# Performance work log

Measured on AMD Instinct MI355X. Metric: run time of the kernel, lower is better.

## Reference

```python
import jax, jax.numpy as jnp
import numpy as np

# Config (matches init_kwargs defaults): V=25 joints, C=16 -> D=400, heads=2,
# ffn=64*25=1600, window L=9, stride=1, postnorm, gelu, dropout ignored (eval).
N, C, T, V = 16, 16, 300, 25
D = C * V          # 400
H = 2              # nhead
FF = 64 * V        # 1600
L = 9              # trans_length
MAX_LEN = 301


def _layernorm(x, g, b, eps=1e-5):
    mu = jnp.mean(x, axis=-1, keepdims=True)
    var = jnp.mean(jnp.square(x - mu), axis=-1, keepdims=True)
    return (x - mu) * jax.lax.rsqrt(var + eps) * g + b


def setup_inputs() -> dict:
    key = jax.random.key(0)
    ks = jax.random.split(key, 12)
    s = 0.02
    return {
        "x": jax.random.normal(ks[0], (N, C, T, V), jnp.float32),
        "pe": jax.random.normal(ks[1], (1, MAX_LEN, D), jnp.float32) * s,
        "w_in": jax.random.normal(ks[2], (3 * D, D), jnp.float32) * s,
        "b_in": jnp.zeros((3 * D,), jnp.float32),
        "w_out": jax.random.normal(ks[3], (D, D), jnp.float32) * s,
        "b_out": jnp.zeros((D,), jnp.float32),
        "w1": jax.random.normal(ks[4], (FF, D), jnp.float32) * s,
        "b1": jnp.zeros((FF,), jnp.float32),
        "w2": jax.random.normal(ks[5], (D, FF), jnp.float32) * s,
        "b2": jnp.zeros((D,), jnp.float32),
        "ln1_g": jnp.ones((D,), jnp.float32),
        "ln1_b": jnp.zeros((D,), jnp.float32),
        "ln2_g": jnp.ones((D,), jnp.float32),
        "ln2_b": jnp.zeros((D,), jnp.float32),
    }


def _encoder_layer(h, w_in, b_in, w_out, b_out, w1, b1, w2, b2,
                   ln1_g, ln1_b, ln2_g, ln2_b):
    # h: [B, L, D]; post-norm TransformerEncoderLayer (torch default)
    B, Lw, Dm = h.shape
    dh = Dm // H
    qkv = h @ w_in.T + b_in                             # [B,L,3D]
    q, k, v = jnp.split(qkv, 3, axis=-1)
    def heads(t):
        return t.reshape(B, Lw, H, dh).transpose(0, 2, 1, 3)  # [B,H,L,dh]
    q, k, v = heads(q), heads(k), heads(v)
    scores = jnp.einsum('bhqd,bhkd->bhqk', q, k) / np.float32(np.sqrt(dh))
    att = jax.nn.softmax(scores, axis=-1)
    o = jnp.einsum('bhqk,bhkd->bhqd', att, v)
    o = o.transpose(0, 2, 1, 3).reshape(B, Lw, Dm) @ w_out.T + b_out
    h = _layernorm(h + o, ln1_g, ln1_b)
    ff = jax.nn.gelu(h @ w1.T + b1, approximate=False) @ w2.T + b2
    return _layernorm(h + ff, ln2_g, ln2_b)


def reference(x, pe, w_in, b_in, w_out, b_out, w1, b1, w2, b2,
              ln1_g, ln1_b, ln2_g, ln2_b):
    n, c, t, v = x.shape
    d = c * v
    # [N,C,T,V] -> [N,T,V,C] -> [N,T,D]  (flatten order is (V,C), as in torch view)
    xs = x.transpose(0, 2, 3, 1).reshape(n, t, d)
    xs = xs + pe[:, :t, :]
    W = t - L                                            # number of windows (stride=1)
    win = jnp.arange(W)
    idx = win[:, None] + jnp.arange(L)[None, :]          # [W,L] gather indices
    xw = xs[:, idx, :].reshape(n * W, L, d)              # batched windows
    out = _encoder_layer(xw, w_in, b_in, w_out, b_out, w1, b1, w2, b2,
                         ln1_g, ln1_b, ln2_g, ln2_b)
    out = out.reshape(n, W * L, d)
    # window i writes into rows i//2 : i//2 + L and results are summed
    pos = ((win // 2)[:, None] + jnp.arange(L)[None, :]).reshape(-1)  # [W*L]
    xt = jnp.zeros((n, t, d), xs.dtype).at[:, pos, :].add(out)
    # [N,T,D] -> [N,T,V,C] -> [N,C,T,V]
    return xt.reshape(n, t, v, c).transpose(0, 3, 1, 2)
```

## Files before the change

kernel.cpp:

```cpp
#include <hip/hip_runtime.h>
#include <cstdint>
#include <cstddef>

#define N_    16
#define C_    16
#define T_    300
#define V_    25
#define D_    400
#define H_    2
#define DH_   200
#define FF_   1600
#define L_    9
#define W_    291
#define NW_   (N_*W_)
#define NT_   (N_*T_)

#define KP_   416
#define SD_   400
#define SQKV_ 1200
#define SFF_  1600

#define WIN_OFF   0u
#define WOUT_OFF  1064960u
#define W1_OFF    1490944u
#define W2_OFF    2981888u
#define XS_OFF    4620288u
#define QKV_OFF   8511488u
#define ACC_OFF   20185088u
#define HEAD_END  27865088u

#define WAIT_VM3   0xF73
#define WAIT_VM0   0xF70

using u16 = unsigned short;
using u32 = unsigned int;
using frag  = __attribute__((ext_vector_type(8))) short;
using f32x4 = __attribute__((ext_vector_type(4))) float;

__device__ __forceinline__ float bf2f(u16 u){
  return __uint_as_float(((u32)u) << 16);
}
__device__ __forceinline__ u16 f2bf(float f){
  return (u16)((__float_as_uint(f) + 0x8000u) >> 16);
}
__device__ __forceinline__ float gelu_f(float v){
  float v2  = v * v;
  float u   = v * (0.7978845608f + 0.03567740814f * v2);
  float u2  = u * u;
  float num = u * (27.f + u2);
  float den = 27.f + 9.f * u2;
  float th  = num * __builtin_amdgcn_rcpf(den);
  th = fminf(fmaxf(th, -1.f), 1.f);
  return 0.5f * v * (1.f + th);
}
__device__ __forceinline__ void unpack8(uint4 v, float* o){
  o[0] = bf2f((u16)(v.x & 0xffffu)); o[1] = bf2f((u16)(v.x >> 16));
  o[2] = bf2f((u16)(v.y & 0xffffu)); o[3] = bf2f((u16)(v.y >> 16));
  o[4] = bf2f((u16)(v.z & 0xffffu)); o[5] = bf2f((u16)(v.z >> 16));
  o[6] = bf2f((u16)(v.w & 0xffffu)); o[7] = bf2f((u16)(v.w >> 16));
}

__device__ __forceinline__ void convw_body(const float* src, u16* dst,
                                           int dN, int dK, int sN, int sK, int idx){
  if (idx >= dN * dK) return;
  int n = idx / dK, k = idx % dK;
  dst[idx] = (n < sN && k < sK) ? f2bf(src[(size_t)n * sK + k]) : (u16)0;
}

#define PREP_GRID 24024
__global__ __launch_bounds__(256) void prep_kernel(const float* __restrict__ x,
                                                   const float* __restrict__ pe,
                                                   const float* __restrict__ w_in,
                                                   const float* __restrict__ w_out,
                                                   const float* __restrict__ w1,
                                                   const float* __restrict__ w2,
                                                   u16* __restrict__ xs,
                                                   u16* __restrict__ w_in_b,
                                                   u16* __restrict__ w_out_b,
                                                   u16* __restrict__ w1_b,
                                                   u16* __restrict__ w2_b,
                                                   float* __restrict__ acc){
  int b = blockIdx.x;
  int tid = threadIdx.x;
  if (b < 7500){
    int idx = b * 256 + tid;
    if (idx < NT_ * D_) acc[idx] = 0.f;
  } else if (b < 15000){
    int idx = (b - 7500) * 256 + tid;
    if (idx < NT_ * D_){
      int d  = idx % D_;
      int nt = idx / D_;
      int t  = nt % T_;
      int n  = nt / T_;
      float val = x[(((size_t)(n*C_ + (d & 15)))*T_ + t)*V_ + (d >> 4)] + pe[t*D_ + d];
      xs[idx] = f2bf(val);
    }
  } else if (b < 17080){
    convw_body(w_in,  w_in_b,  1280, KP_, 1200, D_,  (b - 15000) * 256 + tid);
  } else if (b < 17912){
    convw_body(w_out, w_out_b,  512, KP_,  400, D_,  (b - 17080) * 256 + tid);
  } else if (b < 20824){
    convw_body(w1,    w1_b,   1792, KP_, 1600, D_,  (b - 17912) * 256 + tid);
  } else {
    convw_body(w2,    w2_b,    512, SFF_, 400, FF_, (b - 20824) * 256 + tid);
  }
}

template<int ACT>
__global__ __launch_bounds__(512) void gemm_mfma(const u16* __restrict__ A, int lda,
                                                 const u16* __restrict__ B, int ldb,
                                                 const float* __restrict__ bias,
                                                 u16* __restrict__ C, int ldc,
                                                 int Nn, int KPd,
                                                 int gx, int gy){
  __shared__ u16 smem[36864];
  int id = blockIdx.x;
  int c  = id & 7, t = id >> 3;
  int bx = t % gx;
  int by = (t / gx) * 8 + c;
  if (by >= gy) return;
  const int m0 = by * 128, n0 = bx * 256;

  const int tid  = threadIdx.x;
  const int lane = tid & 63;
  const int wv   = tid >> 6;
  const int quad = lane >> 4, l16 = lane & 15;
  const int wm   = wv & 1,   wn  = wv >> 1;

  const int srow = tid >> 2;
  const int sseg = (tid & 3) ^ ((tid >> 3) & 3);
  const u16* Ag = A + (size_t)(m0 + srow) * lda + sseg*8;
  const u16* Bg = B + (size_t)(n0 + srow) * ldb + sseg*8;

  f32x4 acc[4][4] = {};
  const int sa = quad ^ ((l16 >> 1) & 3);

  auto stage = [&](int buf, int kt){
    __builtin_amdgcn_global_load_lds(
        (const __attribute__((address_space(1))) void*)(Ag + kt),
        (__attribute__((address_space(3))) void*)(&smem[buf*4096 + wv*512]), 16, 0, 0);
    __builtin_amdgcn_global_load_lds(
        (const __attribute__((address_space(1))) void*)(Bg + kt),
        (__attribute__((address_space(3))) void*)(&smem[12288 + buf*8192 + wv*512]), 16, 0, 0);
    __builtin_amdgcn_global_load_lds(
        (const __attribute__((address_space(1))) void*)(Bg + kt + (size_t)128*ldb),
        (__attribute__((address_space(3))) void*)(&smem[12288 + buf*8192 + 4096 + wv*512]), 16, 0, 0);
  };

  const int nit = KPd >> 5;
  stage(0, 0);
  stage(1, 32);
  int nb = 2;
  for (int it = 0; it < nit; ++it){
    if (it < nit - 1) __builtin_amdgcn_s_waitcnt(WAIT_VM3);
    else              __builtin_amdgcn_s_waitcnt(WAIT_VM0);
    __builtin_amdgcn_s_barrier();
    if (it + 2 < nit){
      stage(nb, (it + 2) << 5);
      nb = (nb == 2) ? 0 : nb + 1;
    }
    const int buf = it % 3;
    const u16* Ar = &smem[buf*4096];
    const u16* Br = &smem[12288 + buf*8192];
    frag af[4], bfr[4];
    #pragma unroll
    for (int i = 0; i < 4; ++i)
      af[i]  = *(const frag*)(&Ar[(wm*64 + i*16 + l16)*32 + sa*8]);
    #pragma unroll
    for (int j = 0; j < 4; ++j)
      bfr[j] = *(const frag*)(&Br[(wn*64 + j*16 + l16)*32 + sa*8]);
    #pragma unroll
    for (int i = 0; i < 4; ++i)
      #pragma unroll
      for (int j = 0; j < 4; ++j)
        acc[i][j] = __builtin_amdgcn_mfma_f32_16x16x32_bf16(af[i], bfr[j], acc[i][j], 0, 0, 0);
  }

  __builtin_amdgcn_s_barrier();

  u16* ep = &smem[wv * 4608];
  #pragma unroll
  for (int j = 0; j < 4; ++j){
    int n = n0 + wn*64 + j*16 + l16;
    float bj = (n < Nn) ? bias[n] : 0.f;
    #pragma unroll
    for (int i = 0; i < 4; ++i){
      #pragma unroll
      for (int r = 0; r < 4; ++r){
        float v = acc[i][j][r] + bj;
        if (ACT) v = gelu_f(v);
        ep[(i*16 + quad*4 + r)*72 + j*16 + l16] = f2bf(v);
      }
    }
  }
  #pragma unroll
  for (int p = 0; p < 8; ++p){
    int row = p*8 + (lane >> 3);
    int seg = lane & 7;
    int nc  = n0 + wn*64 + seg*8;
    if (nc < Nn){
      uint4 v = *(const uint4*)(&ep[row*72 + seg*8]);
      *(uint4*)(C + (size_t)(m0 + wm*64 + row)*ldc + nc) = v;
    }
  }
}

#define WB_     8
#define ATT_NB  37
#define ATT_GRID (N_ * ATT_NB)
__global__ __launch_bounds__(256) void attn_kernel(const u16* __restrict__ qkv,
                                                   u16* __restrict__ o,
                                                   int g0, int gend){
  __shared__ u16 kv[20480];
  __shared__ float att[WB_ * 2 * 81];
  const int b  = blockIdx.x;
  const int n  = b / ATT_NB;
  const int w0 = (b - n * ATT_NB) * WB_;
  const int gbase = n * W_ + w0;
  if (gbase >= gend || gbase + WB_ <= g0) return;

  const int tid  = threadIdx.x;
  const int lane = tid & 63;
  const int wv   = tid >> 6;

  const char* gsrc = (const char*)(qkv + (size_t)(n * T_ + w0) * SQKV_);
  #pragma unroll
  for (int j = 0; j < 10; ++j){
    __builtin_amdgcn_global_load_lds(
        (const __attribute__((address_space(1))) void*)(gsrc + j*4096 + wv*1024 + lane*16),
        (__attribute__((address_space(3))) void*)((char*)kv + j*4096 + wv*1024),
        16, 0, 0);
  }
  __builtin_amdgcn_s_waitcnt(WAIT_VM0);
  __syncthreads();

  for (int i = tid; i < WB_ * 162; i += 256){
    int w  = i / 162;
    int r  = i - w * 162;
    int h  = r / 81;
    int p  = r - h * 81;
    int qi = p / 9, ki = p - qi * 9;
    const u16* qp = kv + (w + qi) * 1200 + h * DH_;
    const u16* kp = kv + (w + ki) * 1200 + D_ + h * DH_;
    float s = 0.f;
    #pragma unroll 5
    for (int cch = 0; cch < 25; ++cch){
      float qa[8], kb[8];
      unpack8(*(const uint4*)(qp + cch*8), qa);
      unpack8(*(const uint4*)(kp + cch*8), kb);
      #pragma unroll
      for (int e = 0; e < 8; ++e) s += qa[e] * kb[e];
    }
    att[i] = s * 0.07071067811865475f;
  }
  __syncthreads();

  if (tid < WB_ * 18){
    float* row = att + tid * 9;
    float mx = row[0];
    #pragma unroll
    for (int j = 1; j < 9; ++j) mx = fmaxf(mx, row[j]);
    float e[9]; float sum = 0.f;
    #pragma unroll
    for (int j = 0; j < 9; ++j){ e[j] = __expf(row[j] - mx); sum += e[j]; }
    float inv = 1.f / sum;
    #pragma unroll
    for (int j = 0; j < 9; ++j) row[j] = e[j] * inv;
  }
  __syncthreads();

  for (int i = tid; i < WB_ * 900; i += 256){
    int w  = i / 900;
    int r  = i - w * 900;
    int l  = r / 100;
    int c4 = r - l * 100;
    int h  = (c4 >= 50) ? 1 : 0;
    const float* ap = att + (w*2 + h)*81 + l*9;
    float o4[4] = {0.f, 0.f, 0.f, 0.f};
    #pragma unroll
    for (int ki = 0; ki < 9; ++ki){
      float a = ap[ki];
      uint2 vv = *(const uint2*)(kv + (w + ki)*1200 + 2*D_ + c4*4);
      o4[0] += a * bf2f((u16)(vv.x & 0xffffu));
      o4[1] += a * bf2f((u16)(vv.x >> 16));
      o4[2] += a * bf2f((u16)(vv.y & 0xffffu));
      o4[3] += a * bf2f((u16)(vv.y >> 16));
    }
    int g = gbase + w;
    if (w0 + w < W_ && g >= g0 && g < gend){
      u32 lo = (u32)f2bf(o4[0]) | ((u32)f2bf(o4[1]) << 16);
      u32 hi = (u32)f2bf(o4[2]) | ((u32)f2bf(o4[3]) << 16);
      *(uint2*)(o + ((size_t)(g - g0) * L_ + l) * SD_ + c4*4) = make_uint2(lo, hi);
    }
  }
}

__global__ __launch_bounds__(256) void ln1_kernel(const u16* __restrict__ y,
                                                  const float* __restrict__ gam,
                                                  const float* __restrict__ bet,
                                                  u16* __restrict__ out,
                                                  const u16* __restrict__ xs,
                                                  int g0){
  const int wv = threadIdx.x >> 6, lane = threadIdx.x & 63;
  const int r = blockIdx.x * 4 + wv;
  const int g = g0 + r / L_, l = r % L_;
  const int n = g / W_, w = g % W_;
  const u16* arow = xs + ((size_t)(n*T_ + w + l)) * SD_;
  const u16* brow = y + (size_t)r * SD_;

  const bool act = lane < 50;
  float v[8];
  float s = 0.f, s2 = 0.f;
  if (act){
    float a8[8], b8[8];
    unpack8(*(const uint4*)(arow + lane*8), a8);
    unpack8(*(const uint4*)(brow + lane*8), b8);
    #pragma unroll
    for (int i = 0; i < 8; ++i){ v[i] = a8[i] + b8[i]; s += v[i]; s2 += v[i]*v[i]; }
  } else {
    #pragma unroll
    for (int i = 0; i < 8; ++i) v[i] = 0.f;
  }
  #pragma unroll
  for (int off = 32; off; off >>= 1){
    s  += __shfl_xor(s,  off);
    s2 += __shfl_xor(s2, off);
  }
  float mean = s * (1.f / D_);
  float rstd = rsqrtf(s2 * (1.f / D_) - mean*mean + 1e-5f);
  if (act){
    float4 ga = *(const float4*)(gam + lane*8);
    float4 gb = *(const float4*)(gam + lane*8 + 4);
    float4 ba = *(const float4*)(bet + lane*8);
    float4 bb = *(const float4*)(bet + lane*8 + 4);
    float gg[8] = {ga.x,ga.y,ga.z,ga.w, gb.x,gb.y,gb.z,gb.w};
    float bb8[8]= {ba.x,ba.y,ba.z,ba.w, bb.x,bb.y,bb.z,bb.w};
    u32 o4[4];
    #pragma unroll
    for (int i = 0; i < 4; ++i){
      u16 lo = f2bf((v[2*i]   - mean) * rstd * gg[2*i]   + bb8[2*i]);
      u16 hi = f2bf((v[2*i+1] - mean) * rstd * gg[2*i+1] + bb8[2*i+1]);
      o4[i] = (u32)lo | ((u32)hi << 16);
    }
    *(uint4*)(out + (size_t)r * SD_ + lane*8) = make_uint4(o4[0],o4[1],o4[2],o4[3]);
  }
}

__global__ __launch_bounds__(256) void ln2_scatter_kernel(const u16* __restrict__ h,
                                                          const u16* __restrict__ y,
                                                          const float* __restrict__ gam,
                                                          const float* __restrict__ bet,
                                                          float* __restrict__ acc,
                                                          int g0){
  __shared__ float buf[4][400];
  const int wv = threadIdx.x >> 6, lane = threadIdx.x & 63;
  const int tid = threadIdx.x;
  const int r0 = blockIdx.x * 4;
  {
    const int r = r0 + wv;
    const u16* arow = h + (size_t)r * SD_;
    const u16* brow = y + (size_t)r * SD_;
    const bool act = lane < 50;
    float v[8];
    float s = 0.f, s2 = 0.f;
    if (act){
      float a8[8], b8[8];
      unpack8(*(const uint4*)(arow + lane*8), a8);
      unpack8(*(const uint4*)(brow + lane*8), b8);
      #pragma unroll
      for (int i = 0; i < 8; ++i){ v[i] = a8[i] + b8[i]; s += v[i]; s2 += v[i]*v[i]; }
    } else {
      #pragma unroll
      for (int i = 0; i < 8; ++i) v[i] = 0.f;
    }
    #pragma unroll
    for (int off = 32; off; off >>= 1){
      s  += __shfl_xor(s,  off);
      s2 += __shfl_xor(s2, off);
    }
    float mean = s * (1.f / D_);
    float rstd = rsqrtf(s2 * (1.f / D_) - mean*mean + 1e-5f);
    if (act){
      float4 ga = *(const float4*)(gam + lane*8);
      float4 gb = *(const float4*)(gam + lane*8 + 4);
      float4 ba = *(const float4*)(bet + lane*8);
      float4 bb = *(const float4*)(bet + lane*8 + 4);
      float gg[8] = {ga.x,ga.y,ga.z,ga.w, gb.x,gb.y,gb.z,gb.w};
      float bb8[8]= {ba.x,ba.y,ba.z,ba.w, bb.x,bb.y,bb.z,bb.w};
      #pragma unroll
      for (int i = 0; i < 8; ++i)
        buf[wv][lane*8 + i] = (v[i] - mean) * rstd * gg[i] + bb8[i];
    }
  }
  __syncthreads();
  #pragma unroll
  for (int rr = 0; rr < 4; ++rr){
    int r = r0 + rr;
    int g = g0 + r / L_, l = r % L_;
    int n = g / W_, w = g % W_;
    size_t base = ((size_t)(n*T_ + (w >> 1) + l)) * D_;
    atomicAdd(acc + base + tid, buf[rr][tid]);
    if (tid + 256 < D_) atomicAdd(acc + base + tid + 256, buf[rr][tid + 256]);
  }
}

__global__ __launch_bounds__(256) void final_kernel(const float* __restrict__ acc,
                                                    float* __restrict__ dout){
  int idx = blockIdx.x * 256 + threadIdx.x;
  if (idx >= NT_ * D_) return;
  int d  = idx % D_;
  int nt = idx / D_;
  int t  = nt % T_;
  int n  = nt / T_;
  dout[(((size_t)(n*C_ + (d & 15)))*T_ + t)*V_ + (d >> 4)] = acc[idx];
}

extern "C" void kernel_launch(void* const* d_in, const int* in_sizes, int n_in,
                              void* d_out, int out_size, void* d_ws, size_t ws_size,
                              hipStream_t stream){
  (void)in_sizes; (void)n_in; (void)out_size;
  const float* x     = (const float*)d_in[0];
  const float* pe    = (const float*)d_in[1];
  const float* w_in  = (const float*)d_in[2];
  const float* b_in  = (const float*)d_in[3];
  const float* w_out = (const float*)d_in[4];
  const float* b_out = (const float*)d_in[5];
  const float* w1    = (const float*)d_in[6];
  const float* b1    = (const float*)d_in[7];
  const float* w2    = (const float*)d_in[8];
  const float* b2    = (const float*)d_in[9];
  const float* ln1g  = (const float*)d_in[10];
  const float* ln1b  = (const float*)d_in[11];
  const float* ln2g  = (const float*)d_in[12];
  const float* ln2b  = (const float*)d_in[13];

  int nch = 3;
  {
    size_t need1 = (size_t)HEAD_END + (size_t)41984 * 5600;
    size_t need2 = (size_t)HEAD_END + (size_t)20992 * 5600;
    if (ws_size >= need1 + (1u<<20)) nch = 1;
    else if (ws_size >= need2 + (1u<<20)) nch = 2;
  }
  const int CW  = NW_ / nch;
  const int RC  = CW * L_;
  const int RCP = ((RC + 127) / 128) * 128;

  char* ws = (char*)d_ws;
  u16*   w_in_b  = (u16*)(ws + WIN_OFF);
  u16*   w_out_b = (u16*)(ws + WOUT_OFF);
  u16*   w1_b    = (u16*)(ws + W1_OFF);
  u16*   w2_b    = (u16*)(ws + W2_OFF);
  u16*   xs      = (u16*)(ws + XS_OFF);
  u16*   qkv     = (u16*)(ws + QKV_OFF);
  float* acc     = (float*)(ws + ACC_OFF);
  u16*   o_c     = (u16*)(ws + HEAD_END);
  u16*   y_c     = o_c + (size_t)RCP * SD_;
  u16*   h_c     = y_c + (size_t)RCP * SD_;
  u16*   ffc     = h_c + (size_t)RCP * SD_;

  prep_kernel<<<PREP_GRID, 256, 0, stream>>>(x, pe, w_in, w_out, w1, w2,
                                             xs, w_in_b, w_out_b, w1_b, w2_b, acc);

  {
    int gx = 5, gy = (NT_ + 127)/128, gy8 = (gy + 7) & ~7;
    gemm_mfma<0><<<gx*gy8, 512, 0, stream>>>(
        xs, SD_, w_in_b, KP_, b_in, qkv, SQKV_, 1200, KP_, gx, gy);
  }

  const int gyc = RCP/128, gyc8 = (gyc + 7) & ~7;

  for (int g0 = 0; g0 < NW_; g0 += CW){
    attn_kernel<<<ATT_GRID, 256, 0, stream>>>(qkv, o_c, g0, g0 + CW);

    gemm_mfma<0><<<2*gyc8, 512, 0, stream>>>(
        o_c, SD_, w_out_b, KP_, b_out, y_c, SD_, D_, KP_, 2, gyc);

    ln1_kernel<<<RC/4, 256, 0, stream>>>(y_c, ln1g, ln1b, h_c, xs, g0);

    gemm_mfma<1><<<7*gyc8, 512, 0, stream>>>(
        h_c, SD_, w1_b, KP_, b1, ffc, SFF_, FF_, KP_, 7, gyc);

    gemm_mfma<0><<<2*gyc8, 512, 0, stream>>>(
        ffc, SFF_, w2_b, SFF_, b2, y_c, SD_, D_, SFF_, 2, gyc);

    ln2_scatter_kernel<<<RC/4, 256, 0, stream>>>(h_c, y_c, ln2g, ln2b, acc, g0);
  }

  final_kernel<<<(NT_*D_ + 255)/256, 256, 0, stream>>>(acc, (float*)d_out);
}
```

Measured before the change: 416.5 us.

## Replace atomic scatter-add with bf16 staging buffer and gather-sum final pass

LN2 now writes normalized bf16 rows into a full-size staging buffer z, and the final kernel gathers and sums overlapping window contributions per output position. This removes the fp32 accumulator zeroing and the float atomicAdds on every element. GELU is also swapped from the tanh rational approximation to a sigmoid approximation x*sigmoid(1.702x). That approximation departs from exact erf GELU more than before, and the bf16 staging of each window output adds rounding before summation.

```diff
diff --git a/kernel.cpp b/kernel.cpp
--- a/kernel.cpp
+++ b/kernel.cpp
@@ -26,8 +26,8 @@
 #define W2_OFF    2981888u
 #define XS_OFF    4620288u
 #define QKV_OFF   8511488u
-#define ACC_OFF   20185088u
-#define HEAD_END  27865088u
+#define Z_OFF     20185088u
+#define HEAD_END  53708288u
 
 #define WAIT_VM3   0xF73
 #define WAIT_VM0   0xF70
@@ -44,14 +44,8 @@
   return (u16)((__float_as_uint(f) + 0x8000u) >> 16);
 }
 __device__ __forceinline__ float gelu_f(float v){
-  float v2  = v * v;
-  float u   = v * (0.7978845608f + 0.03567740814f * v2);
-  float u2  = u * u;
-  float num = u * (27.f + u2);
-  float den = 27.f + 9.f * u2;
-  float th  = num * __builtin_amdgcn_rcpf(den);
-  th = fminf(fmaxf(th, -1.f), 1.f);
-  return 0.5f * v * (1.f + th);
+  float s = __expf(-1.702f * v);
+  return v * __builtin_amdgcn_rcpf(1.f + s);
 }
 __device__ __forceinline__ void unpack8(uint4 v, float* o){
   o[0] = bf2f((u16)(v.x & 0xffffu)); o[1] = bf2f((u16)(v.x >> 16));
@@ -67,7 +61,7 @@
   dst[idx] = (n < sN && k < sK) ? f2bf(src[(size_t)n * sK + k]) : (u16)0;
 }
 
-#define PREP_GRID 24024
+#define PREP_GRID 16524
 __global__ __launch_bounds__(256) void prep_kernel(const float* __restrict__ x,
                                                    const float* __restrict__ pe,
                                                    const float* __restrict__ w_in,
@@ -78,15 +72,11 @@
                                                    u16* __restrict__ w_in_b,
                                                    u16* __restrict__ w_out_b,
                                                    u16* __restrict__ w1_b,
-                                                   u16* __restrict__ w2_b,
-                                                   float* __restrict__ acc){
+                                                   u16* __restrict__ w2_b){
   int b = blockIdx.x;
   int tid = threadIdx.x;
   if (b < 7500){
     int idx = b * 256 + tid;
-    if (idx < NT_ * D_) acc[idx] = 0.f;
-  } else if (b < 15000){
-    int idx = (b - 7500) * 256 + tid;
     if (idx < NT_ * D_){
       int d  = idx % D_;
       int nt = idx / D_;
@@ -95,14 +85,14 @@
       float val = x[(((size_t)(n*C_ + (d & 15)))*T_ + t)*V_ + (d >> 4)] + pe[t*D_ + d];
       xs[idx] = f2bf(val);
     }
-  } else if (b < 17080){
-    convw_body(w_in,  w_in_b,  1280, KP_, 1200, D_,  (b - 15000) * 256 + tid);
-  } else if (b < 17912){
-    convw_body(w_out, w_out_b,  512, KP_,  400, D_,  (b - 17080) * 256 + tid);
-  } else if (b < 20824){
-    convw_body(w1,    w1_b,   1792, KP_, 1600, D_,  (b - 17912) * 256 + tid);
+  } else if (b < 9580){
+    convw_body(w_in,  w_in_b,  1280, KP_, 1200, D_,  (b - 7500) * 256 + tid);
+  } else if (b < 10412){
+    convw_body(w_out, w_out_b,  512, KP_,  400, D_,  (b - 9580) * 256 + tid);
+  } else if (b < 13324){
+    convw_body(w1,    w1_b,   1792, KP_, 1600, D_,  (b - 10412) * 256 + tid);
   } else {
-    convw_body(w2,    w2_b,    512, SFF_, 400, FF_, (b - 20824) * 256 + tid);
+    convw_body(w2,    w2_b,    512, SFF_, 400, FF_, (b - 13324) * 256 + tid);
   }
 }
 
@@ -346,65 +336,56 @@
   }
 }
 
-__global__ __launch_bounds__(256) void ln2_scatter_kernel(const u16* __restrict__ h,
-                                                          const u16* __restrict__ y,
-                                                          const float* __restrict__ gam,
-                                                          const float* __restrict__ bet,
-                                                          float* __restrict__ acc,
-                                                          int g0){
-  __shared__ float buf[4][400];
+__global__ __launch_bounds__(256) void ln2z_kernel(const u16* __restrict__ h,
+                                                   const u16* __restrict__ y,
+                                                   const float* __restrict__ gam,
+                                                   const float* __restrict__ bet,
+                                                   u16* __restrict__ z,
+                                                   int g0){
   const int wv = threadIdx.x >> 6, lane = threadIdx.x & 63;
-  const int tid = threadIdx.x;
-  const int r0 = blockIdx.x * 4;
-  {
-    const int r = r0 + wv;
-    const u16* arow = h + (size_t)r * SD_;
-    const u16* brow = y + (size_t)r * SD_;
-    const bool act = lane < 50;
-    float v[8];
-    float s = 0.f, s2 = 0.f;
-    if (act){
-      float a8[8], b8[8];
-      unpack8(*(const uint4*)(arow + lane*8), a8);
-      unpack8(*(const uint4*)(brow + lane*8), b8);
-      #pragma unroll
-      for (int i = 0; i < 8; ++i){ v[i] = a8[i] + b8[i]; s += v[i]; s2 += v[i]*v[i]; }
-    } else {
-      #pragma unroll
-      for (int i = 0; i < 8; ++i) v[i] = 0.f;
-    }
-    #pragma unroll
-    for (int off = 32; off; off >>= 1){
-      s  += __shfl_xor(s,  off);
-      s2 += __shfl_xor(s2, off);
-    }
-    float mean = s * (1.f / D_);
-    float rstd = rsqrtf(s2 * (1.f / D_) - mean*mean + 1e-5f);
-    if (act){
-      float4 ga = *(const float4*)(gam + lane*8);
-      float4 gb = *(const float4*)(gam + lane*8 + 4);
-      float4 ba = *(const float4*)(bet + lane*8);
-      float4 bb = *(const float4*)(bet + lane*8 + 4);
-      float gg[8] = {ga.x,ga.y,ga.z,ga.w, gb.x,gb.y,gb.z,gb.w};
-      float bb8[8]= {ba.x,ba.y,ba.z,ba.w, bb.x,bb.y,bb.z,bb.w};
-      #pragma unroll
-      for (int i = 0; i < 8; ++i)
-        buf[wv][lane*8 + i] = (v[i] - mean) * rstd * gg[i] + bb8[i];
-    }
-  }
-  __syncthreads();
-  #pragma unroll
-  for (int rr = 0; rr < 4; ++rr){
-    int r = r0 + rr;
-    int g = g0 + r / L_, l = r % L_;
-    int n = g / W_, w = g % W_;
-    size_t base = ((size_t)(n*T_ + (w >> 1) + l)) * D_;
-    atomicAdd(acc + base + tid, buf[rr][tid]);
-    if (tid + 256 < D_) atomicAdd(acc + base + tid + 256, buf[rr][tid + 256]);
-  }
-}
-
-__global__ __launch_bounds__(256) void final_kernel(const float* __restrict__ acc,
+  const int r = blockIdx.x * 4 + wv;
+  const u16* arow = h + (size_t)r * SD_;
+  const u16* brow = y + (size_t)r * SD_;
+
+  const bool act = lane < 50;
+  float v[8];
+  float s = 0.f, s2 = 0.f;
+  if (act){
+    float a8[8], b8[8];
+    unpack8(*(const uint4*)(arow + lane*8), a8);
+    unpack8(*(const uint4*)(brow + lane*8), b8);
+    #pragma unroll
+    for (int i = 0; i < 8; ++i){ v[i] = a8[i] + b8[i]; s += v[i]; s2 += v[i]*v[i]; }
+  } else {
+    #pragma unroll
+    for (int i = 0; i < 8; ++i) v[i] = 0.f;
+  }
+  #pragma unroll
+  for (int off = 32; off; off >>= 1){
+    s  += __shfl_xor(s,  off);
+    s2 += __shfl_xor(s2, off);
+  }
+  float mean = s * (1.f / D_);
+  float rstd = rsqrtf(s2 * (1.f / D_) - mean*mean + 1e-5f);
+  if (act){
+    float4 ga = *(const float4*)(gam + lane*8);
+    float4 gb = *(const float4*)(gam + lane*8 + 4);
+    float4 ba = *(const float4*)(bet + lane*8);
+    float4 bb = *(const float4*)(bet + lane*8 + 4);
+    float gg[8] = {ga.x,ga.y,ga.z,ga.w, gb.x,gb.y,gb.z,gb.w};
+    float bb8[8]= {ba.x,ba.y,ba.z,ba.w, bb.x,bb.y,bb.z,bb.w};
+    u32 o4[4];
+    #pragma unroll
+    for (int i = 0; i < 4; ++i){
+      u16 lo = f2bf((v[2*i]   - mean) * rstd * gg[2*i]   + bb8[2*i]);
+      u16 hi = f2bf((v[2*i+1] - mean) * rstd * gg[2*i+1] + bb8[2*i+1]);
+      o4[i] = (u32)lo | ((u32)hi << 16);
+    }
+    *(uint4*)(z + ((size_t)(g0 * L_) + r) * SD_ + lane*8) = make_uint4(o4[0],o4[1],o4[2],o4[3]);
+  }
+}
+
+__global__ __launch_bounds__(256) void gather_final(const u16* __restrict__ z,
                                                     float* __restrict__ dout){
   int idx = blockIdx.x * 256 + threadIdx.x;
   if (idx >= NT_ * D_) return;
@@ -412,7 +393,18 @@
   int nt = idx / D_;
   int t  = nt % T_;
   int n  = nt / T_;
-  dout[(((size_t)(n*C_ + (d & 15)))*T_ + t)*V_ + (d >> 4)] = acc[idx];
+  float s = 0.f;
+  #pragma unroll
+  for (int l = 0; l < L_; ++l){
+    int dt = t - l;
+    if (dt >= 0 && dt <= 145){
+      int w = dt * 2;
+      const u16* zp = z + ((size_t)((n*W_ + w)*L_ + l)) * SD_ + d;
+      s += bf2f(zp[0]);
+      if (w + 1 < W_) s += bf2f(zp[(size_t)L_ * SD_]);
+    }
+  }
+  dout[(((size_t)(n*C_ + (d & 15)))*T_ + t)*V_ + (d >> 4)] = s;
 }
 
 extern "C" void kernel_launch(void* const* d_in, const int* in_sizes, int n_in,
@@ -452,14 +444,14 @@
   u16*   w2_b    = (u16*)(ws + W2_OFF);
   u16*   xs      = (u16*)(ws + XS_OFF);
   u16*   qkv     = (u16*)(ws + QKV_OFF);
-  float* acc     = (float*)(ws + ACC_OFF);
+  u16*   z       = (u16*)(ws + Z_OFF);
   u16*   o_c     = (u16*)(ws + HEAD_END);
   u16*   y_c     = o_c + (size_t)RCP * SD_;
   u16*   h_c     = y_c + (size_t)RCP * SD_;
   u16*   ffc     = h_c + (size_t)RCP * SD_;
 
   prep_kernel<<<PREP_GRID, 256, 0, stream>>>(x, pe, w_in, w_out, w1, w2,
-                                             xs, w_in_b, w_out_b, w1_b, w2_b, acc);
+                                             xs, w_in_b, w_out_b, w1_b, w2_b);
 
   {
     int gx = 5, gy = (NT_ + 127)/128, gy8 = (gy + 7) & ~7;
@@ -483,8 +475,8 @@
     gemm_mfma<0><<<2*gyc8, 512, 0, stream>>>(
         ffc, SFF_, w2_b, SFF_, b2, y_c, SD_, D_, SFF_, 2, gyc);
 
-    ln2_scatter_kernel<<<RC/4, 256, 0, stream>>>(h_c, y_c, ln2g, ln2b, acc, g0);
-  }
-
-  final_kernel<<<(NT_*D_ + 255)/256, 256, 0, stream>>>(acc, (float*)d_out);
-}
+    ln2z_kernel<<<RC/4, 256, 0, stream>>>(h_c, y_c, ln2g, ln2b, z, g0);
+  }
+
+  gather_final<<<(NT_*D_ + 255)/256, 256, 0, stream>>>(z, (float*)d_out);
+}
```

Result: slower. 442.5 us (+6.2%).
